# Kernel optimization log

Hardware: AMD Instinct MI355X
Metric: run time of the kernel (lower is better)

The kernel has to match this reference:

```python
import jax, jax.numpy as jnp
import numpy as np

T, H, NH, NKV, HD, E, K, I = 1024, 2048, 16, 4, 128, 16, 2, 768
EPS = 1e-6
THETA = 10000.0


def setup_inputs() -> dict:
    key = jax.random.key(0)
    ks = jax.random.split(key, 8)
    s = 0.02
    return {
        "hidden_states": jax.random.normal(ks[0], (T, H), jnp.float32),
        "positions": jnp.arange(T, dtype=jnp.int32),
        "w_norm1": jnp.ones((H,), jnp.float32),
        "w_norm2": jnp.ones((H,), jnp.float32),
        "w_qkv": jax.random.normal(ks[1], (H, (NH + 2 * NKV) * HD), jnp.float32) * s,
        "w_qnorm": jnp.ones((HD,), jnp.float32),
        "w_knorm": jnp.ones((HD,), jnp.float32),
        "w_o": jax.random.normal(ks[2], (NH * HD, H), jnp.float32) * s,
        "w_router": jax.random.normal(ks[3], (H, E), jnp.float32) * s,
        "w_gate": jax.random.normal(ks[4], (E, H, I), jnp.float32) * s,
        "w_up": jax.random.normal(ks[5], (E, H, I), jnp.float32) * s,
        "w_down": jax.random.normal(ks[6], (E, I, H), jnp.float32) * s,
    }


def rmsnorm(x, w):
    return x * jax.lax.rsqrt(jnp.mean(x * x, axis=-1, keepdims=True) + EPS) * w


def apply_rope(x, positions):
    # NEOX-style rotary, full head_dim. x: [T, n_heads, HD]
    half = HD // 2
    inv_freq = 1.0 / (THETA ** (jnp.arange(half, dtype=jnp.float32) / half))
    ang = positions.astype(jnp.float32)[:, None] * inv_freq  # [T, half]
    cos = jnp.cos(ang)[:, None, :]
    sin = jnp.sin(ang)[:, None, :]
    x1, x2 = x[..., :half], x[..., half:]
    return jnp.concatenate([x1 * cos - x2 * sin, x2 * cos + x1 * sin], axis=-1)


def reference(hidden_states, positions, w_norm1, w_norm2, w_qkv, w_qnorm, w_knorm,
              w_o, w_router, w_gate, w_up, w_down):
    # prepare_attn: residual = x; h = input_layernorm(x)
    residual = hidden_states
    h = rmsnorm(hidden_states, w_norm1)

    # --- attention (bidirectional, GQA, per-head q/k RMSNorm + RoPE) ---
    qkv = h @ w_qkv
    q, k, v = jnp.split(qkv, [NH * HD, NH * HD + NKV * HD], axis=-1)
    q = rmsnorm(q.reshape(T, NH, HD), w_qnorm)
    k = rmsnorm(k.reshape(T, NKV, HD), w_knorm)
    v = v.reshape(T, NKV, HD)
    q = apply_rope(q, positions)
    k = apply_rope(k, positions)
    rep = NH // NKV
    kf = jnp.repeat(k, rep, axis=1)  # [T, NH, HD]
    vf = jnp.repeat(v, rep, axis=1)
    scores = jnp.einsum('tnd,snd->nts', q, kf) * (HD ** -0.5)  # [NH, T, T]
    p = jax.nn.softmax(scores, axis=-1)
    ctx = jnp.einsum('nts,snd->tnd', p, vf).reshape(T, NH * HD)
    attn_out = ctx @ w_o

    # prepare_mlp: residual = residual + attn_out; h = post_attention_layernorm(residual)
    residual = residual + attn_out
    h = rmsnorm(residual, w_norm2)

    # --- sparse MoE: softmax router, top-k renormalize, SwiGLU experts ---
    logits = h @ w_router
    probs = jax.nn.softmax(logits, axis=-1)
    topw, topi = jax.lax.top_k(probs, K)
    topw = topw / jnp.sum(topw, axis=-1, keepdims=True)
    gates = jnp.zeros((T, E), h.dtype).at[jnp.arange(T)[:, None], topi].set(topw)
    g = jnp.einsum('th,ehi->eti', h, w_gate)
    u = jnp.einsum('th,ehi->eti', h, w_up)
    y = jnp.einsum('eti,eih->eth', jax.nn.silu(g) * u, w_down)
    moe_out = jnp.einsum('eth,te->th', y, gates)

    return moe_out, residual
```

## Files before the change

kernel.cpp:

```cpp
#include <hip/hip_runtime.h>

#define T_    1024
#define H_    2048
#define NH_   16
#define NKV_  4
#define HD_   128
#define E_    16
#define I_    768
#define QKVN  3072

typedef __attribute__((ext_vector_type(8))) short  short8;
typedef __attribute__((ext_vector_type(4))) float  f32x4;
typedef unsigned short u16;

#define LDPA 32
#define LDPB 40

__device__ inline u16 f2bf(float f) {
  unsigned u = __builtin_bit_cast(unsigned, f);
  return (u16)((u + 0x7fffu + ((u >> 16) & 1u)) >> 16);
}
__device__ inline float bf2f(u16 h) {
  unsigned u = ((unsigned)h) << 16;
  return __builtin_bit_cast(float, u);
}

__device__ inline void gll16(const u16* g, u16* l) {
  __builtin_amdgcn_global_load_lds(
      (const __attribute__((address_space(1))) void*)g,
      (__attribute__((address_space(3))) void*)l, 16, 0, 0);
}

__device__ inline float blk_sum(float v, float* lds) {
#pragma unroll
  for (int o = 32; o; o >>= 1) v += __shfl_down(v, o);
  int w = threadIdx.x >> 6;
  __syncthreads();
  if ((threadIdx.x & 63) == 0) lds[w] = v;
  __syncthreads();
  float s = lds[0];
  int nw = blockDim.x >> 6;
  for (int i = 1; i < nw; ++i) s += lds[i];
  return s;
}


struct F4 { float v[4]; };

__device__ inline void wrS(u16* lds, const F4& r) {
  int n = threadIdx.x & 63, kh = (threadIdx.x >> 6) * 4;
  uint2 w;
  w.x = (unsigned)f2bf(r.v[0]) | ((unsigned)f2bf(r.v[1]) << 16);
  w.y = (unsigned)f2bf(r.v[2]) | ((unsigned)f2bf(r.v[3]) << 16);
  *(uint2*)(lds + n * LDPB + kh) = w;
}

template<int SA, int SB>
__device__ inline void mma2(const u16* As, const u16* Bs, f32x4 acc[2][2]) {
  const int lane = threadIdx.x & 63, wv = threadIdx.x >> 6;
  const int wr = wv >> 1, wc = wv & 1;
  const int kk = (lane >> 4) * 8, rr = lane & 15;
  short8 aF[2], bF[2];
#pragma unroll
  for (int m = 0; m < 2; ++m)
    aF[m] = *(const short8*)(As + (wr * 32 + m * 16 + rr) * SA + kk);
#pragma unroll
  for (int n = 0; n < 2; ++n)
    bF[n] = *(const short8*)(Bs + (wc * 32 + n * 16 + rr) * SB + kk);
#pragma unroll
  for (int m = 0; m < 2; ++m)
#pragma unroll
    for (int n = 0; n < 2; ++n)
      acc[m][n] = __builtin_amdgcn_mfma_f32_16x16x32_bf16(aF[m], bF[n], acc[m][n], 0, 0, 0);
}

#define ZERO_ACC(acc) do { \
  _Pragma("unroll") for (int m_ = 0; m_ < 2; ++m_) \
  _Pragma("unroll") for (int n_ = 0; n_ < 2; ++n_) acc[m_][n_] = (f32x4){0.f,0.f,0.f,0.f}; \
} while (0)

#define EPI_ROW(m, r)  (((threadIdx.x >> 6) >> 1) * 32 + (m)*16 + (((threadIdx.x&63) >> 4) * 4) + (r))
#define EPI_COL(n)     ((((threadIdx.x >> 6) & 1) * 32) + (n)*16 + ((threadIdx.x&63) & 15))

template<int NT, class GA, class LB>
__device__ inline void pipeGF(GA ga, LB lb, u16* A0, u16* B0, u16* A1, u16* B1,
                              f32x4 acc[2][2]) {
  F4 b0, b1;
  ga(A0, 0);
  lb(b0, 0); lb(b1, 1);
  wrS(B0, b0);
  if (NT > 2) lb(b0, 2);
#pragma unroll 1
  for (int kt = 0; kt < NT; kt += 2) {
    __syncthreads();
    ga(A1, kt + 1);
    wrS(B1, b1);
    if (kt + 3 < NT) lb(b1, kt + 3);
    mma2<LDPA, LDPB>(A0, B0, acc);
    __syncthreads();
    if (kt + 2 < NT) { ga(A0, kt + 2); wrS(B0, b0); }
    if (kt + 4 < NT) lb(b0, kt + 4);
    mma2<LDPA, LDPB>(A1, B1, acc);
  }
}


__global__ __launch_bounds__(256) void k_rms1(const float* x, const float* w, u16* out) {
  __shared__ float lds[4];
  int t = blockIdx.x, tid = threadIdx.x;
  float v[8]; float ss = 0.f;
#pragma unroll
  for (int i = 0; i < 8; ++i) { v[i] = x[(size_t)t * H_ + tid + 256 * i]; ss += v[i] * v[i]; }
  ss = blk_sum(ss, lds);
  float inv = rsqrtf(ss * (1.f / H_) + 1e-6f);
#pragma unroll
  for (int i = 0; i < 8; ++i)
    out[(size_t)t * H_ + tid + 256 * i] = f2bf(v[i] * inv * w[tid + 256 * i]);
}

__global__ __launch_bounds__(256) void k_rms2(const float* x, const float* w,
                                              float* outf, u16* outb) {
  __shared__ float lds[4];
  int t = blockIdx.x, tid = threadIdx.x;
  float v[8]; float ss = 0.f;
#pragma unroll
  for (int i = 0; i < 8; ++i) { v[i] = x[(size_t)t * H_ + tid + 256 * i]; ss += v[i] * v[i]; }
  ss = blk_sum(ss, lds);
  float inv = rsqrtf(ss * (1.f / H_) + 1e-6f);
#pragma unroll
  for (int i = 0; i < 8; ++i) {
    float r = v[i] * inv * w[tid + 256 * i];
    outf[(size_t)t * H_ + tid + 256 * i] = r;
    outb[(size_t)t * H_ + tid + 256 * i] = f2bf(r);
  }
}

__global__ __launch_bounds__(512) void k_qkv(const u16* h1, const float* wqkv, float* qkv) {
  __shared__ __align__(16) u16 A0[128 * LDPA], A1[128 * LDPA];
  __shared__ __align__(16) u16 B0[64 * LDPB], B1[64 * LDPB];
  int bn = blockIdx.x, bm = blockIdx.y;
  f32x4 acc[2][2]; ZERO_ACC(acc);
  auto ga = [&](u16* As, int kt) {
    gll16(h1 + (size_t)(bm * 128 + (threadIdx.x >> 2)) * H_ + kt * 32 + (threadIdx.x & 3) * 8,
          As + (threadIdx.x & 448) * 8);
  };
  auto lb = [&](F4& r, int kt) {
    int n = threadIdx.x & 63, kh = (threadIdx.x >> 6) * 4;
    const float* src = wqkv + (size_t)(kt * 32 + kh) * QKVN + bn * 64 + n;
#pragma unroll
    for (int j = 0; j < 4; ++j) r.v[j] = src[(size_t)j * QKVN];
  };
  pipeGF<H_ / 32>(ga, lb, A0, B0, A1, B1, acc);
#pragma unroll
  for (int m = 0; m < 2; ++m)
#pragma unroll
    for (int n = 0; n < 2; ++n) {
      f32x4 a = acc[m][n];
#pragma unroll
      for (int r = 0; r < 4; ++r)
        qkv[(size_t)(bm * 128 + EPI_ROW(m, r)) * QKVN + bn * 64 + EPI_COL(n)] = a[r];
    }
}

__global__ __launch_bounds__(256) void k_qkrope(const float* qkv, const int* pos,
                                                const float* wq, const float* wk,
                                                u16* q, u16* kk, u16* vT) {
  __shared__ float cs[64], sn[64];
  int t = blockIdx.x, tid = threadIdx.x, lane = tid & 63, w = tid >> 6;
  if (tid < 64) {
    float fr = expf(-((float)tid / 64.f) * 9.210340371976184f);
    float ang = (float)pos[t] * fr;
    float s_, c_; sincosf(ang, &s_, &c_);
    cs[tid] = c_; sn[tid] = s_;
  }
  __syncthreads();
  const float* row = qkv + (size_t)t * QKVN;
  for (int h = w; h < NH_; h += 4) {
    float x1 = row[h * 128 + lane], x2 = row[h * 128 + 64 + lane];
    float ss = x1 * x1 + x2 * x2;
#pragma unroll
    for (int o = 32; o; o >>= 1) ss += __shfl_down(ss, o);
    ss = __shfl(ss, 0);
    float inv = rsqrtf(ss * (1.f / HD_) + 1e-6f);
    float n1 = x1 * inv * wq[lane], n2 = x2 * inv * wq[64 + lane];
    float o1 = n1 * cs[lane] - n2 * sn[lane];
    float o2 = n2 * cs[lane] + n1 * sn[lane];
    q[(size_t)t * (NH_ * HD_) + h * 128 + lane] = f2bf(o1);
    q[(size_t)t * (NH_ * HD_) + h * 128 + 64 + lane] = f2bf(o2);
  }
  if (w < NKV_) {
    int h = w;
    float x1 = row[2048 + h * 128 + lane], x2 = row[2048 + h * 128 + 64 + lane];
    float ss = x1 * x1 + x2 * x2;
#pragma unroll
    for (int o = 32; o; o >>= 1) ss += __shfl_down(ss, o);
    ss = __shfl(ss, 0);
    float inv = rsqrtf(ss * (1.f / HD_) + 1e-6f);
    float n1 = x1 * inv * wk[lane], n2 = x2 * inv * wk[64 + lane];
    float o1 = n1 * cs[lane] - n2 * sn[lane];
    float o2 = n2 * cs[lane] + n1 * sn[lane];
    kk[((size_t)h * T_ + t) * HD_ + lane] = f2bf(o1);
    kk[((size_t)h * T_ + t) * HD_ + 64 + lane] = f2bf(o2);
    float v1 = row[2560 + h * 128 + lane], v2 = row[2560 + h * 128 + 64 + lane];
    vT[((size_t)(h * 128 + lane)) * T_ + t] = f2bf(v1);
    vT[((size_t)(h * 128 + 64 + lane)) * T_ + t] = f2bf(v2);
  }
}

__global__ __launch_bounds__(256, 1) void k_fattn(const u16* q, const u16* kb,
                                                  const u16* vT, u16* ctx) {
  __shared__ __align__(16) u16 Ks[64 * 136];
  __shared__ __align__(16) u16 Vs[128 * 72];
  __shared__ __align__(16) u16 Ps[4 * 16 * 72];
  int h = blockIdx.x, qt = blockIdx.y;
  int tid = threadIdx.x, lane = tid & 63, wv = tid >> 6;
  int rr = lane & 15, kk = (lane >> 4) * 8;
  const u16* kbh = kb + (size_t)(h >> 2) * T_ * HD_;
  const u16* vTh = vT + (size_t)(h >> 2) * HD_ * T_;
  int q0 = qt * 64 + wv * 16;
  short8 qf[4];
#pragma unroll
  for (int ks = 0; ks < 4; ++ks)
    qf[ks] = *(const short8*)(q + (size_t)(q0 + rr) * (NH_ * HD_) + h * 128 + ks * 32 + kk);
  f32x4 oacc[8];
#pragma unroll
  for (int i = 0; i < 8; ++i) oacc[i] = (f32x4){0.f, 0.f, 0.f, 0.f};
  float lsum[4] = {0.f, 0.f, 0.f, 0.f};
  const float scale = 0.08838834764831845f;
  u16* Pw = Ps + wv * 16 * 72;
#pragma unroll 1
  for (int kv = 0; kv < T_ / 64; ++kv) {
    uint4 kreg[4], vreg[4];
#pragma unroll
    for (int i = 0; i < 4; ++i) {
      int c = tid + 256 * i;
      kreg[i] = *(const uint4*)(kbh + (size_t)(kv * 64 + (c >> 4)) * HD_ + (c & 15) * 8);
      vreg[i] = *(const uint4*)(vTh + (size_t)(c >> 3) * T_ + kv * 64 + (c & 7) * 8);
    }
    __syncthreads();
#pragma unroll
    for (int i = 0; i < 4; ++i) {
      int c = tid + 256 * i;
      *(uint4*)(Ks + (c >> 4) * 136 + (c & 15) * 8) = kreg[i];
      *(uint4*)(Vs + (c >> 3) * 72 + (c & 7) * 8) = vreg[i];
    }
    __syncthreads();
    f32x4 sacc[4];
#pragma unroll
    for (int nf = 0; nf < 4; ++nf) sacc[nf] = (f32x4){0.f, 0.f, 0.f, 0.f};
#pragma unroll
    for (int ks = 0; ks < 4; ++ks)
#pragma unroll
      for (int nf = 0; nf < 4; ++nf) {
        short8 bF = *(const short8*)(Ks + (nf * 16 + rr) * 136 + ks * 32 + kk);
        sacc[nf] = __builtin_amdgcn_mfma_f32_16x16x32_bf16(qf[ks], bF, sacc[nf], 0, 0, 0);
      }
#pragma unroll
    for (int nf = 0; nf < 4; ++nf)
#pragma unroll
      for (int r = 0; r < 4; ++r) {
        float p = __expf(sacc[nf][r] * scale);
        lsum[r] += p;
        Pw[((lane >> 4) * 4 + r) * 72 + nf * 16 + rr] = f2bf(p);
      }
#pragma unroll
    for (int ks2 = 0; ks2 < 2; ++ks2) {
      short8 pa = *(const short8*)(Pw + rr * 72 + ks2 * 32 + kk);
#pragma unroll
      for (int nd = 0; nd < 8; ++nd) {
        short8 bV = *(const short8*)(Vs + (nd * 16 + rr) * 72 + ks2 * 32 + kk);
        oacc[nd] = __builtin_amdgcn_mfma_f32_16x16x32_bf16(pa, bV, oacc[nd], 0, 0, 0);
      }
    }
  }
#pragma unroll
  for (int r = 0; r < 4; ++r) {
#pragma unroll
    for (int o = 1; o < 16; o <<= 1) lsum[r] += __shfl_xor(lsum[r], o);
    lsum[r] = 1.f / lsum[r];
  }
#pragma unroll
  for (int nd = 0; nd < 8; ++nd)
#pragma unroll
    for (int r = 0; r < 4; ++r)
      ctx[(size_t)(q0 + (lane >> 4) * 4 + r) * (NH_ * HD_) + h * 128 + nd * 16 + rr] =
          f2bf(oacc[nd][r] * lsum[r]);
}

__global__ __launch_bounds__(512) void k_wo(const u16* ctx, const float* wo,
                                            const float* hs, float* resid) {
  __shared__ __align__(16) u16 A0[128 * LDPA], A1[128 * LDPA];
  __shared__ __align__(16) u16 B0[64 * LDPB], B1[64 * LDPB];
  int bn = blockIdx.x, bm = blockIdx.y;
  f32x4 acc[2][2]; ZERO_ACC(acc);
  auto ga = [&](u16* As, int kt) {
    gll16(ctx + (size_t)(bm * 128 + (threadIdx.x >> 2)) * H_ + kt * 32 + (threadIdx.x & 3) * 8,
          As + (threadIdx.x & 448) * 8);
  };
  auto lb = [&](F4& r, int kt) {
    int n = threadIdx.x & 63, kh = (threadIdx.x >> 6) * 4;
    const float* src = wo + (size_t)(kt * 32 + kh) * H_ + bn * 64 + n;
#pragma unroll
    for (int j = 0; j < 4; ++j) r.v[j] = src[(size_t)j * H_];
  };
  pipeGF<H_ / 32>(ga, lb, A0, B0, A1, B1, acc);
#pragma unroll
  for (int m = 0; m < 2; ++m)
#pragma unroll
    for (int n = 0; n < 2; ++n) {
      f32x4 a = acc[m][n];
#pragma unroll
      for (int r = 0; r < 4; ++r) {
        size_t idx = (size_t)(bm * 128 + EPI_ROW(m, r)) * H_ + bn * 64 + EPI_COL(n);
        resid[idx] = a[r] + hs[idx];
      }
    }
}

__global__ __launch_bounds__(256) void k_router(const float* h2f, const float* wr_,
                                                int* topi, float* topw, int* cnt) {
  __shared__ float xs[H_];
  __shared__ float red[4][16];
  __shared__ float lg[16];
  int t = blockIdx.x, tid = threadIdx.x;
#pragma unroll
  for (int i = 0; i < 8; ++i) xs[tid + 256 * i] = h2f[(size_t)t * H_ + tid + 256 * i];
  __syncthreads();
  int e = tid & 15, p = tid >> 4;
  float s = 0.f;
  int b0 = p * 128;
  for (int i = 0; i < 128; ++i) s += xs[b0 + i] * wr_[(size_t)(b0 + i) * E_ + e];
  s += __shfl_down(s, 32);
  s += __shfl_down(s, 16);
  int lane = tid & 63, w = tid >> 6;
  if (lane < 16) red[w][lane] = s;
  __syncthreads();
  if (tid < 16) lg[tid] = red[0][tid] + red[1][tid] + red[2][tid] + red[3][tid];
  __syncthreads();
  if (tid == 0) {
    float l1 = -1e30f; int e1 = 0;
    for (int i = 0; i < E_; ++i) if (lg[i] > l1) { l1 = lg[i]; e1 = i; }
    float l2 = -1e30f; int e2 = 0;
    for (int i = 0; i < E_; ++i) if (i != e1 && lg[i] > l2) { l2 = lg[i]; e2 = i; }
    float d = __expf(l2 - l1);
    float w1 = 1.f / (1.f + d), w2 = d / (1.f + d);
    topi[2 * t] = e1; topi[2 * t + 1] = e2;
    topw[2 * t] = w1; topw[2 * t + 1] = w2;
    atomicAdd(&cnt[e1], 1);
    atomicAdd(&cnt[e2], 1);
  }
}

__global__ void k_scan(const int* cnt, int* basearr) {
  if (threadIdx.x == 0) {
    int b = 0;
    for (int e = 0; e < E_; ++e) { basearr[e] = b; b += cnt[e]; }
    basearr[E_] = b;
  }
}

__global__ __launch_bounds__(256) void k_assign(const int* topi, const float* topw,
                                                const int* basearr, int* posc,
                                                int* tok, float* wslot) {
  int t = blockIdx.x * 256 + threadIdx.x;
  if (t < T_) {
#pragma unroll
    for (int j = 0; j < 2; ++j) {
      int e = topi[2 * t + j];
      int p = atomicAdd(&posc[e], 1);
      int s = basearr[e] + p;
      tok[s] = t;
      wslot[s] = topw[2 * t + j];
    }
  }
}

__global__ __launch_bounds__(512) void k_gateup(const u16* h2b,
                                                const float* wg, const float* wu,
                                                const int* cnt, const int* basearr, const int* tok,
                                                u16* act) {
  __shared__ __align__(16) u16 A0[128 * LDPA], A1[128 * LDPA];
  __shared__ __align__(16) u16 B0[64 * LDPB], B1[64 * LDPB];
  __shared__ int gat_s[128];
  int e = blockIdx.x;
  int c = cnt[e];
  int mt = blockIdx.z;
  if (mt * 128 >= c) return;
  int basee = basearr[e];
  int gmax = c - mt * 128;
  int n0 = blockIdx.y * 32;
  int tid = threadIdx.x;
  if (tid < 128) {
    int r = mt * 128 + tid;
    gat_s[tid] = (r < c) ? tok[basee + r] : tok[basee];
  }
  __syncthreads();
  int grow = gat_s[tid >> 2];
  const float* Bg = wg + (size_t)e * H_ * I_;
  const float* Bu = wu + (size_t)e * H_ * I_;
  f32x4 acc[2][2]; ZERO_ACC(acc);
  auto ga = [&](u16* As, int kt) {
    gll16(h2b + (size_t)grow * H_ + kt * 32 + (tid & 3) * 8, As + (tid & 448) * 8);
  };
  auto lb = [&](F4& r, int kt) {
    int cidx = tid & 63, kh = (tid >> 6) * 4;
    int fn = cidx >> 4;
    const float* base = (fn & 1) ? Bu : Bg;
    int col = n0 + (fn >> 1) * 16 + (cidx & 15);
    const float* src = base + (size_t)(kt * 32 + kh) * I_ + col;
#pragma unroll
    for (int j = 0; j < 4; ++j) r.v[j] = src[(size_t)j * I_];
  };
  pipeGF<H_ / 32>(ga, lb, A0, B0, A1, B1, acc);
  int slot0 = basee + mt * 128;
  int col = n0 + ((tid >> 6) & 1) * 16 + ((tid & 63) & 15);
#pragma unroll
  for (int m = 0; m < 2; ++m) {
#pragma unroll
    for (int r = 0; r < 4; ++r) {
      int row = EPI_ROW(m, r);
      if (row >= gmax) continue;
      float g = acc[m][0][r], u = acc[m][1][r];
      float sg = g / (1.f + __expf(-g));
      act[(size_t)(slot0 + row) * I_ + col] = f2bf(sg * u);
    }
  }
}

__global__ __launch_bounds__(512) void k_down(const u16* act, const float* wd,
                                              const int* cnt, const int* basearr,
                                              const int* tok, const float* wslot,
                                              float* moe) {
  __shared__ __align__(16) u16 A0[128 * LDPA], A1[128 * LDPA];
  __shared__ __align__(16) u16 B0[64 * LDPB], B1[64 * LDPB];
  int e = blockIdx.y;
  int c = cnt[e];
  int mt = blockIdx.z;
  if (mt * 128 >= c) return;
  int basee = basearr[e];
  int gmax = c - mt * 128;
  int slot0 = basee + mt * 128;
  int n0 = blockIdx.x * 64;
  const u16* Ap = act + (size_t)slot0 * I_;
  const float* Bp = wd + (size_t)e * I_ * H_;
  f32x4 acc[2][2]; ZERO_ACC(acc);
  auto ga = [&](u16* As, int kt) {
    gll16(Ap + (size_t)(threadIdx.x >> 2) * I_ + kt * 32 + (threadIdx.x & 3) * 8,
          As + (threadIdx.x & 448) * 8);
  };
  auto lb = [&](F4& r, int kt) {
    int n = threadIdx.x & 63, kh = (threadIdx.x >> 6) * 4;
    const float* src = Bp + (size_t)(kt * 32 + kh) * H_ + n0 + n;
#pragma unroll
    for (int j = 0; j < 4; ++j) r.v[j] = src[(size_t)j * H_];
  };
  pipeGF<I_ / 32>(ga, lb, A0, B0, A1, B1, acc);
#pragma unroll
  for (int m = 0; m < 2; ++m)
#pragma unroll
    for (int n = 0; n < 2; ++n) {
      f32x4 a = acc[m][n];
#pragma unroll
      for (int r = 0; r < 4; ++r) {
        int row = EPI_ROW(m, r);
        if (row >= gmax) continue;
        int col = EPI_COL(n);
        int slot = slot0 + row;
        float wgt = wslot[slot];
        int tk = tok[slot];
        atomicAdd(&moe[(size_t)tk * H_ + n0 + col], a[r] * wgt);
      }
    }
}

extern "C" void kernel_launch(void* const* d_in, const int* in_sizes, int n_in,
                              void* d_out, int out_size, void* d_ws, size_t ws_size,
                              hipStream_t stream) {
  const float* hs    = (const float*)d_in[0];
  const int*   pos   = (const int*)d_in[1];
  const float* wn1   = (const float*)d_in[2];
  const float* wn2   = (const float*)d_in[3];
  const float* wqkv  = (const float*)d_in[4];
  const float* wqn   = (const float*)d_in[5];
  const float* wkn   = (const float*)d_in[6];
  const float* wo    = (const float*)d_in[7];
  const float* wrt   = (const float*)d_in[8];
  const float* wg    = (const float*)d_in[9];
  const float* wu    = (const float*)d_in[10];
  const float* wd    = (const float*)d_in[11];
  float* out = (float*)d_out;
  float* moe_out = out;
  float* resid   = out + (size_t)T_ * H_;

  char* ws = (char*)d_ws;
  size_t off = 0;
  auto alloc = [&](size_t bytes) { size_t r = off; off = (off + bytes + 255) & ~(size_t)255; return r; };
  u16*   h1   = (u16*)  (ws + alloc((size_t)T_ * H_ * 2));
  float* qkv  = (float*)(ws + alloc((size_t)T_ * QKVN * 4));
  u16*   q    = (u16*)  (ws + alloc((size_t)T_ * NH_ * HD_ * 2));
  u16*   kb   = (u16*)  (ws + alloc((size_t)NKV_ * T_ * HD_ * 2));
  u16*   vT   = (u16*)  (ws + alloc((size_t)NKV_ * HD_ * T_ * 2));
  u16*   ctx  = (u16*)  (ws + alloc((size_t)T_ * NH_ * HD_ * 2));
  float* h2f  = (float*)(ws + alloc((size_t)T_ * H_ * 4));
  u16*   h2b  = (u16*)  (ws + alloc((size_t)T_ * H_ * 2));
  u16*   act  = (u16*)  (ws + alloc((size_t)(2 * T_ + 256) * I_ * 2));
  int*   topi = (int*)  (ws + alloc((size_t)T_ * 2 * 4));
  float* topw = (float*)(ws + alloc((size_t)T_ * 2 * 4));
  int*   cnt  = (int*)  (ws + alloc(32 * 4));
  int*   posc = cnt + 16;
  int*   base = (int*)  (ws + alloc(32 * 4));
  int*   tok  = (int*)  (ws + alloc((size_t)(2 * T_ + 128) * 4));
  float* wsl  = (float*)(ws + alloc((size_t)(2 * T_ + 128) * 4));
  (void)ws_size; (void)in_sizes; (void)n_in; (void)out_size;

  hipMemsetAsync(moe_out, 0, (size_t)T_ * H_ * 4, stream);
  hipMemsetAsync(cnt, 0, 32 * 4, stream);

  k_rms1<<<T_, 256, 0, stream>>>(hs, wn1, h1);
  k_qkv<<<dim3(QKVN / 64, T_ / 128), 512, 0, stream>>>(h1, wqkv, qkv);
  k_qkrope<<<T_, 256, 0, stream>>>(qkv, pos, wqn, wkn, q, kb, vT);
  k_fattn<<<dim3(NH_, T_ / 64), 256, 0, stream>>>(q, kb, vT, ctx);
  k_wo<<<dim3(H_ / 64, T_ / 128), 512, 0, stream>>>(ctx, wo, hs, resid);
  k_rms2<<<T_, 256, 0, stream>>>(resid, wn2, h2f, h2b);
  k_router<<<T_, 256, 0, stream>>>(h2f, wrt, topi, topw, cnt);
  k_scan<<<1, 64, 0, stream>>>(cnt, base);
  k_assign<<<4, 256, 0, stream>>>(topi, topw, base, posc, tok, wsl);
  k_gateup<<<dim3(E_, I_ / 32, T_ / 128), 512, 0, stream>>>(h2b, wg, wu, cnt, base, tok, act);
  k_down<<<dim3(H_ / 64, E_, T_ / 128), 512, 0, stream>>>(act, wd, cnt, base, tok, wsl, moe_out);
}
```

Before: 366.1 us.

## Split attention over KV into four partitions with separate reduction kernel

```diff
diff --git a/kernel.cpp b/kernel.cpp
--- a/kernel.cpp
+++ b/kernel.cpp
@@ -207,12 +207,12 @@
   }
 }
 
-__global__ __launch_bounds__(256, 1) void k_fattn(const u16* q, const u16* kb,
-                                                  const u16* vT, u16* ctx) {
+__global__ __launch_bounds__(256) void k_fattn(const u16* q, const u16* kb,
+                                               const u16* vT, float* opart, float* lpart) {
   __shared__ __align__(16) u16 Ks[64 * 136];
   __shared__ __align__(16) u16 Vs[128 * 72];
   __shared__ __align__(16) u16 Ps[4 * 16 * 72];
-  int h = blockIdx.x, qt = blockIdx.y;
+  int h = blockIdx.x, qt = blockIdx.y, kvs = blockIdx.z;
   int tid = threadIdx.x, lane = tid & 63, wv = tid >> 6;
   int rr = lane & 15, kk = (lane >> 4) * 8;
   const u16* kbh = kb + (size_t)(h >> 2) * T_ * HD_;
@@ -229,20 +229,33 @@
   const float scale = 0.08838834764831845f;
   u16* Pw = Ps + wv * 16 * 72;
 #pragma unroll 1
-  for (int kv = 0; kv < T_ / 64; ++kv) {
-    uint4 kreg[4], vreg[4];
-#pragma unroll
-    for (int i = 0; i < 4; ++i) {
-      int c = tid + 256 * i;
-      kreg[i] = *(const uint4*)(kbh + (size_t)(kv * 64 + (c >> 4)) * HD_ + (c & 15) * 8);
-      vreg[i] = *(const uint4*)(vTh + (size_t)(c >> 3) * T_ + kv * 64 + (c & 7) * 8);
-    }
+  for (int kv = kvs * 4; kv < kvs * 4 + 4; ++kv) {
     __syncthreads();
-#pragma unroll
-    for (int i = 0; i < 4; ++i) {
-      int c = tid + 256 * i;
-      *(uint4*)(Ks + (c >> 4) * 136 + (c & 15) * 8) = kreg[i];
-      *(uint4*)(Vs + (c >> 3) * 72 + (c & 7) * 8) = vreg[i];
+    {
+      uint4 kreg[4];
+#pragma unroll
+      for (int i = 0; i < 4; ++i) {
+        int c = tid + 256 * i;
+        kreg[i] = *(const uint4*)(kbh + (size_t)(kv * 64 + (c >> 4)) * HD_ + (c & 15) * 8);
+      }
+#pragma unroll
+      for (int i = 0; i < 4; ++i) {
+        int c = tid + 256 * i;
+        *(uint4*)(Ks + (c >> 4) * 136 + (c & 15) * 8) = kreg[i];
+      }
+    }
+    {
+      uint4 vreg[4];
+#pragma unroll
+      for (int i = 0; i < 4; ++i) {
+        int c = tid + 256 * i;
+        vreg[i] = *(const uint4*)(vTh + (size_t)(c >> 3) * T_ + kv * 64 + (c & 7) * 8);
+      }
+#pragma unroll
+      for (int i = 0; i < 4; ++i) {
+        int c = tid + 256 * i;
+        *(uint4*)(Vs + (c >> 3) * 72 + (c & 7) * 8) = vreg[i];
+      }
     }
     __syncthreads();
     f32x4 sacc[4];
@@ -277,14 +290,36 @@
   for (int r = 0; r < 4; ++r) {
 #pragma unroll
     for (int o = 1; o < 16; o <<= 1) lsum[r] += __shfl_xor(lsum[r], o);
-    lsum[r] = 1.f / lsum[r];
-  }
+  }
+  if ((lane & 15) == 0) {
+#pragma unroll
+    for (int r = 0; r < 4; ++r)
+      lpart[((size_t)kvs * NH_ + h) * T_ + q0 + (lane >> 4) * 4 + r] = lsum[r];
+  }
+  float* op = opart + (size_t)kvs * T_ * (NH_ * HD_);
 #pragma unroll
   for (int nd = 0; nd < 8; ++nd)
 #pragma unroll
     for (int r = 0; r < 4; ++r)
-      ctx[(size_t)(q0 + (lane >> 4) * 4 + r) * (NH_ * HD_) + h * 128 + nd * 16 + rr] =
-          f2bf(oacc[nd][r] * lsum[r]);
+      op[(size_t)(q0 + (lane >> 4) * 4 + r) * (NH_ * HD_) + h * 128 + nd * 16 + rr] =
+          oacc[nd][r];
+}
+
+__global__ __launch_bounds__(256) void k_attnfin(const float* opart, const float* lpart,
+                                                 u16* ctx) {
+  int t = blockIdx.x, tid = threadIdx.x;
+#pragma unroll
+  for (int i = 0; i < 8; ++i) {
+    int idx = tid + 256 * i;
+    int h = idx >> 7;
+    float l = 0.f, o = 0.f;
+#pragma unroll
+    for (int s = 0; s < 4; ++s) {
+      l += lpart[((size_t)s * NH_ + h) * T_ + t];
+      o += opart[(size_t)s * T_ * (NH_ * HD_) + (size_t)t * (NH_ * HD_) + idx];
+    }
+    ctx[(size_t)t * (NH_ * HD_) + idx] = f2bf(o / l);
+  }
 }
 
 __global__ __launch_bounds__(512) void k_wo(const u16* ctx, const float* wo,
@@ -495,22 +530,24 @@
   char* ws = (char*)d_ws;
   size_t off = 0;
   auto alloc = [&](size_t bytes) { size_t r = off; off = (off + bytes + 255) & ~(size_t)255; return r; };
-  u16*   h1   = (u16*)  (ws + alloc((size_t)T_ * H_ * 2));
-  float* qkv  = (float*)(ws + alloc((size_t)T_ * QKVN * 4));
-  u16*   q    = (u16*)  (ws + alloc((size_t)T_ * NH_ * HD_ * 2));
-  u16*   kb   = (u16*)  (ws + alloc((size_t)NKV_ * T_ * HD_ * 2));
-  u16*   vT   = (u16*)  (ws + alloc((size_t)NKV_ * HD_ * T_ * 2));
-  u16*   ctx  = (u16*)  (ws + alloc((size_t)T_ * NH_ * HD_ * 2));
-  float* h2f  = (float*)(ws + alloc((size_t)T_ * H_ * 4));
-  u16*   h2b  = (u16*)  (ws + alloc((size_t)T_ * H_ * 2));
-  u16*   act  = (u16*)  (ws + alloc((size_t)(2 * T_ + 256) * I_ * 2));
-  int*   topi = (int*)  (ws + alloc((size_t)T_ * 2 * 4));
-  float* topw = (float*)(ws + alloc((size_t)T_ * 2 * 4));
-  int*   cnt  = (int*)  (ws + alloc(32 * 4));
-  int*   posc = cnt + 16;
-  int*   base = (int*)  (ws + alloc(32 * 4));
-  int*   tok  = (int*)  (ws + alloc((size_t)(2 * T_ + 128) * 4));
-  float* wsl  = (float*)(ws + alloc((size_t)(2 * T_ + 128) * 4));
+  u16*   h1    = (u16*)  (ws + alloc((size_t)T_ * H_ * 2));
+  float* qkv   = (float*)(ws + alloc((size_t)T_ * QKVN * 4));
+  u16*   q     = (u16*)  (ws + alloc((size_t)T_ * NH_ * HD_ * 2));
+  u16*   kb    = (u16*)  (ws + alloc((size_t)NKV_ * T_ * HD_ * 2));
+  u16*   vT    = (u16*)  (ws + alloc((size_t)NKV_ * HD_ * T_ * 2));
+  u16*   ctx   = (u16*)  (ws + alloc((size_t)T_ * NH_ * HD_ * 2));
+  float* opart = (float*)(ws + alloc((size_t)4 * T_ * NH_ * HD_ * 4));
+  float* lpart = (float*)(ws + alloc((size_t)4 * NH_ * T_ * 4));
+  float* h2f   = (float*)(ws + alloc((size_t)T_ * H_ * 4));
+  u16*   h2b   = (u16*)  (ws + alloc((size_t)T_ * H_ * 2));
+  u16*   act   = (u16*)  (ws + alloc((size_t)(2 * T_ + 256) * I_ * 2));
+  int*   topi  = (int*)  (ws + alloc((size_t)T_ * 2 * 4));
+  float* topw  = (float*)(ws + alloc((size_t)T_ * 2 * 4));
+  int*   cnt   = (int*)  (ws + alloc(32 * 4));
+  int*   posc  = cnt + 16;
+  int*   base  = (int*)  (ws + alloc(32 * 4));
+  int*   tok   = (int*)  (ws + alloc((size_t)(2 * T_ + 128) * 4));
+  float* wsl   = (float*)(ws + alloc((size_t)(2 * T_ + 128) * 4));
   (void)ws_size; (void)in_sizes; (void)n_in; (void)out_size;
 
   hipMemsetAsync(moe_out, 0, (size_t)T_ * H_ * 4, stream);
@@ -519,7 +556,8 @@
   k_rms1<<<T_, 256, 0, stream>>>(hs, wn1, h1);
   k_qkv<<<dim3(QKVN / 64, T_ / 128), 512, 0, stream>>>(h1, wqkv, qkv);
   k_qkrope<<<T_, 256, 0, stream>>>(qkv, pos, wqn, wkn, q, kb, vT);
-  k_fattn<<<dim3(NH_, T_ / 64), 256, 0, stream>>>(q, kb, vT, ctx);
+  k_fattn<<<dim3(NH_, T_ / 64, 4), 256, 0, stream>>>(q, kb, vT, opart, lpart);
+  k_attnfin<<<T_, 256, 0, stream>>>(opart, lpart, ctx);
   k_wo<<<dim3(H_ / 64, T_ / 128), 512, 0, stream>>>(ctx, wo, hs, resid);
   k_rms2<<<T_, 256, 0, stream>>>(resid, wn2, h2f, h2b);
   k_router<<<T_, 256, 0, stream>>>(h2f, wrt, topi, topw, cnt);
```

Result: faster. 331.3 us, median of 2 (-9.5%).
